# Optimization experiments

Hardware: AMD Instinct MI355X
Metric: run time of the kernel (lower is better)

The kernel has to match this reference:

```python
import jax, jax.numpy as jnp
import numpy as np

B, T, D = 4096, 200, 64
NEG_INF = -(2.0 ** 32) + 1.0  # matches tf paddings constant


def setup_inputs() -> dict:
    key = jax.random.key(0)
    ks = jax.random.split(key, 12)
    queries = jax.random.normal(ks[0], (B, D), dtype=jnp.float32)
    keys = jax.random.normal(ks[1], (B, T, D), dtype=jnp.float32)
    keys_length = jax.random.randint(ks[2], (B,), 0, 200, dtype=jnp.int32)
    # attention MLP params (glorot-ish scale)
    W1 = jax.random.normal(ks[3], (4 * D, 16), dtype=jnp.float32) * (1.0 / np.sqrt(4 * D))
    b1 = jnp.zeros((16,), dtype=jnp.float32)
    W2 = jax.random.normal(ks[4], (16, 8), dtype=jnp.float32) * (1.0 / np.sqrt(16))
    b2 = jnp.zeros((8,), dtype=jnp.float32)
    W3 = jax.random.normal(ks[5], (8, 1), dtype=jnp.float32) * (1.0 / np.sqrt(8))
    b3 = jnp.zeros((1,), dtype=jnp.float32)
    W4 = jax.random.normal(ks[6], (D, D), dtype=jnp.float32) * (1.0 / np.sqrt(D))
    b4 = jnp.zeros((D,), dtype=jnp.float32)
    return {"queries": queries, "keys": keys, "keys_length": keys_length,
            "W1": W1, "b1": b1, "W2": W2, "b2": b2, "W3": W3, "b3": b3,
            "W4": W4, "b4": b4}


def reference(queries, keys, keys_length, W1, b1, W2, b2, W3, b3, W4, b4):
    Bq, Tq, Dq = keys.shape
    # tile queries across time: [B, T, D]
    q = jnp.broadcast_to(queries[:, None, :], (Bq, Tq, Dq))
    # DIN feature construction: [B, T, 4D]
    din_all = jnp.concatenate([q, keys, q - keys, q * keys], axis=-1)
    # tiny MLP scorer
    x = jax.nn.sigmoid(jnp.einsum('btf,fh->bth', din_all, W1) + b1)
    x = jax.nn.sigmoid(jnp.einsum('bth,hk->btk', x, W2) + b2)
    scores = (jnp.einsum('btk,ko->bto', x, W3) + b3)[..., 0]  # [B, T]
    # mask invalid history positions
    mask = jnp.arange(Tq, dtype=keys_length.dtype)[None, :] < keys_length[:, None]
    scores = jnp.where(mask, scores, NEG_INF)
    scores = scores / (Dq ** 0.5)  # scaling applied after masking, as in tf code
    attn = jax.nn.softmax(scores, axis=-1)  # [B, T]
    out = jnp.einsum('bt,btd->bd', attn, keys)  # weighted sum of keys
    out = out @ W4 + b4  # [B, D]
    return out
```

## Files before the change

### kernel.cpp

```cpp
#include <hip/hip_runtime.h>
#include <math.h>

#define TT 200
#define DD 64
#define H1STR 20

typedef __attribute__((ext_vector_type(8))) short bf16x8;
typedef __attribute__((ext_vector_type(4))) float f32x4;

__device__ __forceinline__ float sigmoidf_(float x) {
    return 1.0f / (1.0f + __expf(-x));
}
__device__ __forceinline__ short f2bf(float x) {
    unsigned u = __float_as_uint(x);
    u += 0x7fff + ((u >> 16) & 1);
    return (short)(u >> 16);
}
__device__ __forceinline__ float bf2f(short s) {
    return __uint_as_float(((unsigned)(unsigned short)s) << 16);
}
__device__ __forceinline__ void build_hi(float4 v0, float4 v1, bf16x8& hi) {
    float xs[8] = {v0.x, v0.y, v0.z, v0.w, v1.x, v1.y, v1.z, v1.w};
    #pragma unroll
    for (int j = 0; j < 8; j++) hi[j] = f2bf(xs[j]);
}

__global__ __launch_bounds__(256) void din_attn_kernel(
    const float* __restrict__ queries,
    const float* __restrict__ keys,
    const int*   __restrict__ keys_length,
    const float* __restrict__ W1,
    const float* __restrict__ b1,
    const float* __restrict__ W2,
    const float* __restrict__ b2,
    const float* __restrict__ W3,
    const float* __restrict__ b3,
    const float* __restrict__ W4,
    const float* __restrict__ b4,
    float* __restrict__ out)
{
    __shared__ __align__(16) short H1s[4][208 * H1STR];
    __shared__ __align__(16) float scoresS[4][200];
    __shared__ __align__(16) float tmpv[4][64];

    const int tid  = threadIdx.x;
    const int w    = tid >> 6;
    const int lane = tid & 63;
    const int m16  = lane & 15;
    const int quad = lane >> 4;
    const int b    = blockIdx.x * 4 + w;
    const int len  = keys_length[b];
    const float* kb = keys + (size_t)b * (TT * DD);

    short* h1p = &H1s[w][0];
    float* scp = &scoresS[w][0];
    float* tvp = &tmpv[w][0];

    const float* kp0 = kb + m16 * 64 + quad * 8;
    float4 c0 = *(const float4*)(kp0);
    float4 c1 = *(const float4*)(kp0 + 4);
    float4 c2 = *(const float4*)(kp0 + 32);
    float4 c3 = *(const float4*)(kp0 + 36);

    bf16x8 Bh0, Bl0, Bh1, Bl1;
    float cvec;
    {
        const int d0 = quad * 8;
        const float* qb = queries + b * 64 + d0;
        float4 qv0 = *(const float4*)(qb);
        float4 qv1 = *(const float4*)(qb + 4);
        float4 qv2 = *(const float4*)(qb + 32);
        float4 qv3 = *(const float4*)(qb + 36);
        float qa[8] = {qv0.x, qv0.y, qv0.z, qv0.w, qv1.x, qv1.y, qv1.z, qv1.w};
        float qc[8] = {qv2.x, qv2.y, qv2.z, qv2.w, qv3.x, qv3.y, qv3.z, qv3.w};
        float cp = 0.0f;
        #pragma unroll
        for (int j = 0; j < 8; j++) {
            {
                const int d = d0 + j;
                float a  = W1[(0   + d) * 16 + m16];
                float bb = W1[(64  + d) * 16 + m16];
                float cc = W1[(128 + d) * 16 + m16];
                float dd = W1[(192 + d) * 16 + m16];
                float mv = bb - cc + qa[j] * dd;
                cp = fmaf(qa[j], a + cc, cp);
                short hi = f2bf(mv);
                Bh0[j] = hi;
                Bl0[j] = f2bf(mv - bf2f(hi));
            }
            {
                const int d = d0 + j + 32;
                float a  = W1[(0   + d) * 16 + m16];
                float bb = W1[(64  + d) * 16 + m16];
                float cc = W1[(128 + d) * 16 + m16];
                float dd = W1[(192 + d) * 16 + m16];
                float mv = bb - cc + qc[j] * dd;
                cp = fmaf(qc[j], a + cc, cp);
                short hi = f2bf(mv);
                Bh1[j] = hi;
                Bl1[j] = f2bf(mv - bf2f(hi));
            }
        }
        cp += __shfl_xor(cp, 16, 64);
        cp += __shfl_xor(cp, 32, 64);
        cvec = b1[m16] + cp;
    }

    #pragma unroll 1
    for (int tile = 0; tile < 13; tile++) {
        float4 n0, n1, n2, n3;
        if (tile < 12) {
            int trow = (tile + 1) * 16 + m16;
            if (trow > TT - 1) trow = TT - 1;
            const float* kp = kb + trow * 64 + quad * 8;
            n0 = *(const float4*)(kp);
            n1 = *(const float4*)(kp + 4);
            n2 = *(const float4*)(kp + 32);
            n3 = *(const float4*)(kp + 36);
        }
        bf16x8 ah0, ah1;
        build_hi(c0, c1, ah0);
        build_hi(c2, c3, ah1);
        f32x4 acc = {0.f, 0.f, 0.f, 0.f};
        acc = __builtin_amdgcn_mfma_f32_16x16x32_bf16(ah0, Bh0, acc, 0, 0, 0);
        acc = __builtin_amdgcn_mfma_f32_16x16x32_bf16(ah0, Bl0, acc, 0, 0, 0);
        acc = __builtin_amdgcn_mfma_f32_16x16x32_bf16(ah1, Bh1, acc, 0, 0, 0);
        acc = __builtin_amdgcn_mfma_f32_16x16x32_bf16(ah1, Bl1, acc, 0, 0, 0);
        const int rb = tile * 16 + quad * 4;
        h1p[(rb + 0) * H1STR + m16] = f2bf(sigmoidf_(acc[0] + cvec));
        h1p[(rb + 1) * H1STR + m16] = f2bf(sigmoidf_(acc[1] + cvec));
        h1p[(rb + 2) * H1STR + m16] = f2bf(sigmoidf_(acc[2] + cvec));
        h1p[(rb + 3) * H1STR + m16] = f2bf(sigmoidf_(acc[3] + cvec));
        c0 = n0; c1 = n1; c2 = n2; c3 = n3;
    }

    float w3v[8], b2v[8];
    #pragma unroll
    for (int k = 0; k < 8; k++) { w3v[k] = W3[k]; b2v[k] = b2[k]; }
    const float b3v = b3[0];

    float sc[4];
    #pragma unroll
    for (int i = 0; i < 4; i++) {
        int t  = lane + 64 * i;
        int tr = (t > 207) ? 207 : t;
        const uint2* hrow = (const uint2*)&h1p[tr * H1STR];
        uint2 u0 = hrow[0], u1 = hrow[1], u2 = hrow[2], u3 = hrow[3];
        float hv[16];
        hv[0]  = __uint_as_float(u0.x << 16); hv[1]  = __uint_as_float(u0.x & 0xffff0000u);
        hv[2]  = __uint_as_float(u0.y << 16); hv[3]  = __uint_as_float(u0.y & 0xffff0000u);
        hv[4]  = __uint_as_float(u1.x << 16); hv[5]  = __uint_as_float(u1.x & 0xffff0000u);
        hv[6]  = __uint_as_float(u1.y << 16); hv[7]  = __uint_as_float(u1.y & 0xffff0000u);
        hv[8]  = __uint_as_float(u2.x << 16); hv[9]  = __uint_as_float(u2.x & 0xffff0000u);
        hv[10] = __uint_as_float(u2.y << 16); hv[11] = __uint_as_float(u2.y & 0xffff0000u);
        hv[12] = __uint_as_float(u3.x << 16); hv[13] = __uint_as_float(u3.x & 0xffff0000u);
        hv[14] = __uint_as_float(u3.y << 16); hv[15] = __uint_as_float(u3.y & 0xffff0000u);

        float s2[8];
        #pragma unroll
        for (int k = 0; k < 8; k++) s2[k] = b2v[k];
        #pragma unroll
        for (int h = 0; h < 16; h++) {
            const float hh = hv[h];
            const float4* w2r = (const float4*)&W2[h * 8];
            float4 wa = w2r[0], wb = w2r[1];
            s2[0] = fmaf(hh, wa.x, s2[0]);
            s2[1] = fmaf(hh, wa.y, s2[1]);
            s2[2] = fmaf(hh, wa.z, s2[2]);
            s2[3] = fmaf(hh, wa.w, s2[3]);
            s2[4] = fmaf(hh, wb.x, s2[4]);
            s2[5] = fmaf(hh, wb.y, s2[5]);
            s2[6] = fmaf(hh, wb.z, s2[6]);
            s2[7] = fmaf(hh, wb.w, s2[7]);
        }
        float s3 = b3v;
        #pragma unroll
        for (int k = 0; k < 8; k++) s3 = fmaf(sigmoidf_(s2[k]), w3v[k], s3);
        if (t >= len) s3 = -4294967295.0f;
        sc[i] = s3 * 0.125f;
    }

    float m = fmaxf(fmaxf(sc[0], sc[1]), fmaxf(sc[2], sc[3]));
    #pragma unroll
    for (int off = 32; off >= 1; off >>= 1) m = fmaxf(m, __shfl_xor(m, off, 64));
    float p[4];
    float ssum = 0.0f;
    #pragma unroll
    for (int i = 0; i < 4; i++) {
        int t = lane + 64 * i;
        p[i] = (t < TT) ? __expf(sc[i] - m) : 0.0f;
        ssum += p[i];
    }
    #pragma unroll
    for (int off = 32; off >= 1; off >>= 1) ssum += __shfl_xor(ssum, off, 64);
    const float inv = 1.0f / ssum;
    #pragma unroll
    for (int i = 0; i < 4; i++) {
        int t = lane + 64 * i;
        if (t < TT) scp[t] = p[i];
    }

    float ws = 0.0f;
    const float4* sp4 = (const float4*)scp;
    #pragma unroll 5
    for (int g = 0; g < 50; g++) {
        float4 pv = sp4[g];
        const float* kq = kb + (g * 4) * 64 + lane;
        ws = fmaf(pv.x, kq[0],   ws);
        ws = fmaf(pv.y, kq[64],  ws);
        ws = fmaf(pv.z, kq[128], ws);
        ws = fmaf(pv.w, kq[192], ws);
    }
    tvp[lane] = ws * inv;

    float o = b4[lane];
    const float4* tv4 = (const float4*)tvp;
    #pragma unroll 4
    for (int g = 0; g < 16; g++) {
        float4 tv = tv4[g];
        const float* w4q = W4 + (g * 4) * 64 + lane;
        o = fmaf(tv.x, w4q[0],   o);
        o = fmaf(tv.y, w4q[64],  o);
        o = fmaf(tv.z, w4q[128], o);
        o = fmaf(tv.w, w4q[192], o);
    }
    out[(size_t)b * 64 + lane] = o;
}

extern "C" void kernel_launch(void* const* d_in, const int* in_sizes, int n_in,
                              void* d_out, int out_size, void* d_ws, size_t ws_size,
                              hipStream_t stream) {
    const float* queries     = (const float*)d_in[0];
    const float* keys        = (const float*)d_in[1];
    const int*   keys_length = (const int*)  d_in[2];
    const float* W1 = (const float*)d_in[3];
    const float* b1 = (const float*)d_in[4];
    const float* W2 = (const float*)d_in[5];
    const float* b2 = (const float*)d_in[6];
    const float* W3 = (const float*)d_in[7];
    const float* b3 = (const float*)d_in[8];
    const float* W4 = (const float*)d_in[9];
    const float* b4 = (const float*)d_in[10];
    float* out = (float*)d_out;

    const int Bn = in_sizes[2];
    din_attn_kernel<<<Bn / 4, 256, 0, stream>>>(
        queries, keys, keys_length, W1, b1, W2, b2, W3, b3, W4, b4, out);
}
```

Measured before the change: 321.7 us.

## Fuse MLP tail, softmax and weighted key sum into the streaming tile loop

Layers 2 and 3 of the scorer, the exponentiation and the weighted key sum now run inside the per-tile loop. The weighted sum reuses the key values already held in registers for the MFMA, so keys are not read from global memory a second time. Softmax drops the max subtraction, which is safe because the scores are bounded by the sigmoid outputs, and it handles len==0 as a uniform distribution. Launch changes to one 64-thread wave per batch row with minimal shared memory. The tradeoff is that the 16 scorer rows are computed redundantly by all four quads, and cross-lane shuffle reductions are added at the end.

```diff
diff --git a/kernel.cpp b/kernel.cpp
--- a/kernel.cpp
+++ b/kernel.cpp
@@ -2,7 +2,6 @@
 #include <math.h>
 
 #define TT 200
-#define DD 64
 #define H1STR 20
 
 typedef __attribute__((ext_vector_type(8))) short bf16x8;
@@ -25,7 +24,7 @@
     for (int j = 0; j < 8; j++) hi[j] = f2bf(xs[j]);
 }
 
-__global__ __launch_bounds__(256) void din_attn_kernel(
+__global__ __launch_bounds__(64, 4) void din_attn_kernel(
     const float* __restrict__ queries,
     const float* __restrict__ keys,
     const int*   __restrict__ keys_length,
@@ -39,22 +38,15 @@
     const float* __restrict__ b4,
     float* __restrict__ out)
 {
-    __shared__ __align__(16) short H1s[4][208 * H1STR];
-    __shared__ __align__(16) float scoresS[4][200];
-    __shared__ __align__(16) float tmpv[4][64];
-
-    const int tid  = threadIdx.x;
-    const int w    = tid >> 6;
-    const int lane = tid & 63;
+    __shared__ __align__(8)  short h1t[16 * H1STR];
+    __shared__ __align__(16) float tmpv[64];
+
+    const int lane = threadIdx.x;
     const int m16  = lane & 15;
     const int quad = lane >> 4;
-    const int b    = blockIdx.x * 4 + w;
+    const int b    = blockIdx.x;
     const int len  = keys_length[b];
-    const float* kb = keys + (size_t)b * (TT * DD);
-
-    short* h1p = &H1s[w][0];
-    float* scp = &scoresS[w][0];
-    float* tvp = &tmpv[w][0];
+    const float* kb = keys + (size_t)b * (TT * 64);
 
     const float* kp0 = kb + m16 * 64 + quad * 8;
     float4 c0 = *(const float4*)(kp0);
@@ -106,6 +98,16 @@
         cvec = b1[m16] + cp;
     }
 
+    float w3v[8], b2v[8];
+    #pragma unroll
+    for (int k = 0; k < 8; k++) { w3v[k] = W3[k]; b2v[k] = b2[k]; }
+    const float b3v = b3[0];
+
+    float ws0[8], ws1[8];
+    #pragma unroll
+    for (int j = 0; j < 8; j++) { ws0[j] = 0.0f; ws1[j] = 0.0f; }
+    float ssum = 0.0f;
+
     #pragma unroll 1
     for (int tile = 0; tile < 13; tile++) {
         float4 n0, n1, n2, n3;
@@ -118,6 +120,7 @@
             n2 = *(const float4*)(kp + 32);
             n3 = *(const float4*)(kp + 36);
         }
+
         bf16x8 ah0, ah1;
         build_hi(c0, c1, ah0);
         build_hi(c2, c3, ah1);
@@ -126,25 +129,13 @@
         acc = __builtin_amdgcn_mfma_f32_16x16x32_bf16(ah0, Bl0, acc, 0, 0, 0);
         acc = __builtin_amdgcn_mfma_f32_16x16x32_bf16(ah1, Bh1, acc, 0, 0, 0);
         acc = __builtin_amdgcn_mfma_f32_16x16x32_bf16(ah1, Bl1, acc, 0, 0, 0);
-        const int rb = tile * 16 + quad * 4;
-        h1p[(rb + 0) * H1STR + m16] = f2bf(sigmoidf_(acc[0] + cvec));
-        h1p[(rb + 1) * H1STR + m16] = f2bf(sigmoidf_(acc[1] + cvec));
-        h1p[(rb + 2) * H1STR + m16] = f2bf(sigmoidf_(acc[2] + cvec));
-        h1p[(rb + 3) * H1STR + m16] = f2bf(sigmoidf_(acc[3] + cvec));
-        c0 = n0; c1 = n1; c2 = n2; c3 = n3;
-    }
-
-    float w3v[8], b2v[8];
-    #pragma unroll
-    for (int k = 0; k < 8; k++) { w3v[k] = W3[k]; b2v[k] = b2[k]; }
-    const float b3v = b3[0];
-
-    float sc[4];
-    #pragma unroll
-    for (int i = 0; i < 4; i++) {
-        int t  = lane + 64 * i;
-        int tr = (t > 207) ? 207 : t;
-        const uint2* hrow = (const uint2*)&h1p[tr * H1STR];
+
+        #pragma unroll
+        for (int r = 0; r < 4; r++)
+            h1t[(quad * 4 + r) * H1STR + m16] = f2bf(sigmoidf_(acc[r] + cvec));
+        __asm__ volatile("s_waitcnt lgkmcnt(0)" ::: "memory");
+
+        const uint2* hrow = (const uint2*)&h1t[m16 * H1STR];
         uint2 u0 = hrow[0], u1 = hrow[1], u2 = hrow[2], u3 = hrow[3];
         float hv[16];
         hv[0]  = __uint_as_float(u0.x << 16); hv[1]  = __uint_as_float(u0.x & 0xffff0000u);
@@ -176,45 +167,56 @@
         float s3 = b3v;
         #pragma unroll
         for (int k = 0; k < 8; k++) s3 = fmaf(sigmoidf_(s2[k]), w3v[k], s3);
-        if (t >= len) s3 = -4294967295.0f;
-        sc[i] = s3 * 0.125f;
-    }
-
-    float m = fmaxf(fmaxf(sc[0], sc[1]), fmaxf(sc[2], sc[3]));
-    #pragma unroll
-    for (int off = 32; off >= 1; off >>= 1) m = fmaxf(m, __shfl_xor(m, off, 64));
-    float p[4];
-    float ssum = 0.0f;
-    #pragma unroll
-    for (int i = 0; i < 4; i++) {
-        int t = lane + 64 * i;
-        p[i] = (t < TT) ? __expf(sc[i] - m) : 0.0f;
-        ssum += p[i];
-    }
-    #pragma unroll
-    for (int off = 32; off >= 1; off >>= 1) ssum += __shfl_xor(ssum, off, 64);
+        const float sc = s3 * 0.125f;
+
+        const int t = tile * 16 + m16;
+        float p;
+        if (len == 0) p = (t < TT) ? 1.0f : 0.0f;
+        else          p = (t < len) ? __expf(sc) : 0.0f;
+        ssum += p;
+
+        ws0[0] = fmaf(p, c0.x, ws0[0]);
+        ws0[1] = fmaf(p, c0.y, ws0[1]);
+        ws0[2] = fmaf(p, c0.z, ws0[2]);
+        ws0[3] = fmaf(p, c0.w, ws0[3]);
+        ws0[4] = fmaf(p, c1.x, ws0[4]);
+        ws0[5] = fmaf(p, c1.y, ws0[5]);
+        ws0[6] = fmaf(p, c1.z, ws0[6]);
+        ws0[7] = fmaf(p, c1.w, ws0[7]);
+        ws1[0] = fmaf(p, c2.x, ws1[0]);
+        ws1[1] = fmaf(p, c2.y, ws1[1]);
+        ws1[2] = fmaf(p, c2.z, ws1[2]);
+        ws1[3] = fmaf(p, c2.w, ws1[3]);
+        ws1[4] = fmaf(p, c3.x, ws1[4]);
+        ws1[5] = fmaf(p, c3.y, ws1[5]);
+        ws1[6] = fmaf(p, c3.z, ws1[6]);
+        ws1[7] = fmaf(p, c3.w, ws1[7]);
+
+        c0 = n0; c1 = n1; c2 = n2; c3 = n3;
+    }
+
+    #pragma unroll
+    for (int mask = 1; mask <= 8; mask <<= 1) {
+        ssum += __shfl_xor(ssum, mask, 64);
+        #pragma unroll
+        for (int j = 0; j < 8; j++) {
+            ws0[j] += __shfl_xor(ws0[j], mask, 64);
+            ws1[j] += __shfl_xor(ws1[j], mask, 64);
+        }
+    }
     const float inv = 1.0f / ssum;
-    #pragma unroll
-    for (int i = 0; i < 4; i++) {
-        int t = lane + 64 * i;
-        if (t < TT) scp[t] = p[i];
-    }
-
-    float ws = 0.0f;
-    const float4* sp4 = (const float4*)scp;
-    #pragma unroll 5
-    for (int g = 0; g < 50; g++) {
-        float4 pv = sp4[g];
-        const float* kq = kb + (g * 4) * 64 + lane;
-        ws = fmaf(pv.x, kq[0],   ws);
-        ws = fmaf(pv.y, kq[64],  ws);
-        ws = fmaf(pv.z, kq[128], ws);
-        ws = fmaf(pv.w, kq[192], ws);
-    }
-    tvp[lane] = ws * inv;
+
+    #pragma unroll
+    for (int j = 0; j < 8; j++) {
+        if (m16 == j) {
+            tmpv[quad * 8 + j]      = ws0[j] * inv;
+            tmpv[32 + quad * 8 + j] = ws1[j] * inv;
+        }
+    }
+    __asm__ volatile("s_waitcnt lgkmcnt(0)" ::: "memory");
 
     float o = b4[lane];
-    const float4* tv4 = (const float4*)tvp;
+    const float4* tv4 = (const float4*)tmpv;
     #pragma unroll 4
     for (int g = 0; g < 16; g++) {
         float4 tv = tv4[g];
@@ -244,6 +246,6 @@
     float* out = (float*)d_out;
 
     const int Bn = in_sizes[2];
-    din_attn_kernel<<<Bn / 4, 256, 0, stream>>>(
+    din_attn_kernel<<<Bn, 64, 0, stream>>>(
         queries, keys, keys_length, W1, b1, W2, b2, W3, b3, W4, b4, out);
 }
```

Result: no change. 319.3 us (-0.8%).
